# Kernel optimization log

Hardware: AMD Instinct MI355X
Metric: run time of the kernel (lower is better)

The kernel has to match this reference:

```python
import jax, jax.numpy as jnp
import numpy as np

B, T, C, H = 4, 1024, 1024, 16
HS = C // H  # head_size = 64
EPS = 1e-5


def layer_norm(x, w, b):
    mu = jnp.mean(x, axis=-1, keepdims=True)
    var = jnp.mean(jnp.square(x - mu), axis=-1, keepdims=True)
    return (x - mu) * jax.lax.rsqrt(var + EPS) * w + b


def setup_inputs() -> dict:
    key = jax.random.key(0)
    ks = jax.random.split(key, 12)
    s = 0.02
    return {
        "x": jax.random.normal(ks[0], (B, T, C), jnp.float32),
        "ln1_w": jnp.ones((C,), jnp.float32),
        "ln1_b": jnp.zeros((C,), jnp.float32),
        "Wk": jax.random.normal(ks[1], (H, C, HS), jnp.float32) * s,
        "Wq": jax.random.normal(ks[2], (H, C, HS), jnp.float32) * s,
        "Wv": jax.random.normal(ks[3], (H, C, HS), jnp.float32) * s,
        "Wo": jax.random.normal(ks[4], (C, C), jnp.float32) * s,
        "bo": jnp.zeros((C,), jnp.float32),
        "ln2_w": jnp.ones((C,), jnp.float32),
        "ln2_b": jnp.zeros((C,), jnp.float32),
        "W1": jax.random.normal(ks[5], (C, 4 * C), jnp.float32) * s,
        "b1": jnp.zeros((4 * C,), jnp.float32),
        "prelu_a": jnp.asarray(0.25, jnp.float32),
        "W2": jax.random.normal(ks[6], (4 * C, C), jnp.float32) * s,
        "b2": jnp.zeros((C,), jnp.float32),
    }


def reference(x, ln1_w, ln1_b, Wk, Wq, Wv, Wo, bo, ln2_w, ln2_b, W1, b1, prelu_a, W2, b2):
    # --- self-attention branch (pre-LN) ---
    h = layer_norm(x, ln1_w, ln1_b)  # [B,T,C]
    k = jnp.einsum('btc,hcd->bhtd', h, Wk)
    q = jnp.einsum('btc,hcd->bhtd', h, Wq)
    v = jnp.einsum('btc,hcd->bhtd', h, Wv)
    # NOTE: source computes k @ q^T (not q @ k^T) scaled by n_embd**-0.5
    wei = jnp.einsum('bhtd,bhsd->bhts', k, q) * (C ** -0.5)  # [B,H,T,T]
    causal = jnp.tril(jnp.ones((T, T), bool))
    wei = jnp.where(causal, wei, -jnp.inf)
    wei = jax.nn.softmax(wei, axis=-1)
    out = jnp.einsum('bhts,bhsd->bthd', wei, v).reshape(B, T, C)
    out = out @ Wo + bo
    x = x + out
    # --- feed-forward branch (pre-LN) ---
    h2 = layer_norm(x, ln2_w, ln2_b)
    f = h2 @ W1 + b1
    f = jnp.where(f > 0, f, prelu_a * f)  # PReLU, single scalar param
    f = f @ W2 + b2
    return x + f
```

## Files before the change

kernel.cpp:

```cpp
#include <hip/hip_runtime.h>


typedef __bf16 bf16_t;
typedef __attribute__((ext_vector_type(8))) __bf16 bfx8;
typedef __attribute__((ext_vector_type(4))) __bf16 bfx4;
typedef __attribute__((ext_vector_type(4))) float f32x4;
typedef __attribute__((ext_vector_type(8))) unsigned short u16x8;
typedef unsigned int u32;

#define MFMA_BF16(a, b, c) __builtin_amdgcn_mfma_f32_16x16x32_bf16((a), (b), (c), 0, 0, 0)
#define GLOAD_LDS16(g, l)                                                     \
  __builtin_amdgcn_global_load_lds((__attribute__((address_space(1))) void*)(g), \
                                   (__attribute__((address_space(3))) void*)(l), 16, 0, 0)
#define BARX()                      \
  __builtin_amdgcn_s_barrier();     \
  __builtin_amdgcn_sched_barrier(0)
#define VMW6()                                     \
  asm volatile("s_waitcnt vmcnt(6)" ::: "memory"); \
  __builtin_amdgcn_sched_barrier(0)
#define VMW0()                                     \
  asm volatile("s_waitcnt vmcnt(0)" ::: "memory"); \
  __builtin_amdgcn_sched_barrier(0)

__global__ __launch_bounds__(256) void ln_kernel(const float* __restrict__ x,
                                                 const float* __restrict__ w,
                                                 const float* __restrict__ b,
                                                 bf16_t* __restrict__ out) {
  const int row = blockIdx.x;
  const int tid = threadIdx.x;
  const float4 v = reinterpret_cast<const float4*>(x + (size_t)row * 1024)[tid];
  float s = v.x + v.y + v.z + v.w;
  float s2 = v.x * v.x + v.y * v.y + v.z * v.z + v.w * v.w;
#pragma unroll
  for (int off = 1; off < 64; off <<= 1) {
    s += __shfl_xor(s, off);
    s2 += __shfl_xor(s2, off);
  }
  __shared__ float red[8];
  const int wv = tid >> 6;
  if ((tid & 63) == 0) {
    red[wv] = s;
    red[4 + wv] = s2;
  }
  __syncthreads();
  s = red[0] + red[1] + red[2] + red[3];
  s2 = red[4] + red[5] + red[6] + red[7];
  const float mu = s * (1.0f / 1024.0f);
  const float rs = rsqrtf(s2 * (1.0f / 1024.0f) - mu * mu + 1e-5f);
  const float4 wv4 = reinterpret_cast<const float4*>(w)[tid];
  const float4 bv4 = reinterpret_cast<const float4*>(b)[tid];
  bfx4 o;
  o[0] = (bf16_t)((v.x - mu) * rs * wv4.x + bv4.x);
  o[1] = (bf16_t)((v.y - mu) * rs * wv4.y + bv4.y);
  o[2] = (bf16_t)((v.z - mu) * rs * wv4.z + bv4.z);
  o[3] = (bf16_t)((v.w - mu) * rs * wv4.w + bv4.w);
  reinterpret_cast<bfx4*>(out + (size_t)row * 1024)[tid] = o;
}

__device__ __forceinline__ void tc_body(const float* __restrict__ in,
                                        bf16_t* __restrict__ out, int K, int N, int k0,
                                        int n0, float (*tile)[65], int t) {
  const int rl = t >> 4, cl = (t & 15) * 4;
#pragma unroll
  for (int p = 0; p < 4; ++p) {
    const int r = p * 16 + rl;
    const float4 v = *reinterpret_cast<const float4*>(in + (size_t)(k0 + r) * N + n0 + cl);
    tile[r][cl] = v.x;
    tile[r][cl + 1] = v.y;
    tile[r][cl + 2] = v.z;
    tile[r][cl + 3] = v.w;
  }
  __syncthreads();
#pragma unroll
  for (int p = 0; p < 2; ++p) {
    const int idx = p * 256 + t;
    const int n = idx >> 3, kc = (idx & 7) * 8;
    bfx8 o;
#pragma unroll
    for (int i = 0; i < 8; ++i) o[i] = (bf16_t)tile[kc + i][n];
    *reinterpret_cast<bfx8*>(out + (size_t)(n0 + n) * K + k0 + kc) = o;
  }
}

__global__ __launch_bounds__(256) void transpose_cast(const float* __restrict__ in,
                                                      bf16_t* __restrict__ out, int K,
                                                      int N) {
  __shared__ float tile[64][65];
  tc_body(in, out, K, N, blockIdx.x * 64, blockIdx.y * 64, tile, threadIdx.x);
}

__global__ __launch_bounds__(256) void transpose_qkv(const float* __restrict__ Wq,
                                                     const float* __restrict__ Wk,
                                                     const float* __restrict__ Wv,
                                                     bf16_t* __restrict__ out) {
  __shared__ float tile[64][65];
  const int z = blockIdx.y;
  const int sel = z >> 4, h = z & 15;
  const float* in = ((sel == 0) ? Wq : (sel == 1) ? Wk : Wv) + h * 65536;
  bf16_t* o = out + (size_t)sel * 1048576 + h * 65536;
  tc_body(in, o, 1024, 64, blockIdx.x * 64, 0, tile, threadIdx.x);
}

enum { EPI_QKV = 0, EPI_WO = 1 };

template <int EPI, int BM, int BN, int NT>
__global__ __launch_bounds__(NT, 2) void gemm_bt(
    const bf16_t* __restrict__ A, const bf16_t* __restrict__ BT,
    const float* __restrict__ bias, const float* __restrict__ res,
    float* __restrict__ outf, bf16_t* __restrict__ ob0, bf16_t* __restrict__ ob1,
    bf16_t* __restrict__ ob2, int K, int N) {
  constexpr int WM = 2;
  constexpr int WN = NT / 64 / WM;
  constexpr int MF = BM / WM / 16;
  constexpr int NF = BN / WN / 16;
  constexpr int ACH = BM * 64 / (NT * 8);
  constexpr int BCH = BN * 64 / (NT * 8);
  constexpr int LOADS = ACH + BCH;
  static_assert(LOADS == 8 || LOADS == 6, "add a vmcnt case");
  __shared__ __align__(16) bf16_t sA[2][BM * 64];
  __shared__ __align__(16) bf16_t sB[2][BN * 64];
  const int tid = threadIdx.x;
  const int lane = tid & 63;
  const int w = tid >> 6;
  const int wr = w / WN, wc = w % WN;
  const int g = lane >> 4, l15 = lane & 15;
  const int row0 = blockIdx.x * BM, col0 = blockIdx.y * BN;
  const int rowbase = row0 + wr * (BM / WM);
  const int colbase = wc * (BN / WN);

  f32x4 acc[MF][NF] = {};

  auto stage = [&](int k0, int buf) {
#pragma unroll
    for (int j = 0; j < ACH; ++j) {
      const int chunk = j * NT + tid;
      const int r = chunk >> 3, c = chunk & 7;
      GLOAD_LDS16(A + (size_t)(row0 + r) * K + k0 + ((c ^ (r & 7)) * 8),
                  sA[buf] + chunk * 8);
    }
#pragma unroll
    for (int j = 0; j < BCH; ++j) {
      const int chunk = j * NT + tid;
      const int r = chunk >> 3, c = chunk & 7;
      GLOAD_LDS16(BT + (size_t)(col0 + r) * K + k0 + ((c ^ (r & 7)) * 8),
                  sB[buf] + chunk * 8);
    }
  };

  stage(0, 0);
  const int nk = K >> 6;
  for (int t = 0; t < nk; ++t) {
    const int cur = t & 1;
    if (t + 1 < nk) {
      stage((t + 1) << 6, cur ^ 1);
      __builtin_amdgcn_sched_barrier(0);
      if constexpr (LOADS == 8)
        asm volatile("s_waitcnt vmcnt(8)" ::: "memory");
      else
        asm volatile("s_waitcnt vmcnt(6)" ::: "memory");
    } else {
      __builtin_amdgcn_sched_barrier(0);
      asm volatile("s_waitcnt vmcnt(0)" ::: "memory");
    }
    __builtin_amdgcn_s_barrier();
    __builtin_amdgcn_sched_barrier(0);
    const bf16_t* __restrict__ pA = sA[cur];
    const bf16_t* __restrict__ pB = sB[cur];
#pragma unroll
    for (int kk = 0; kk < 2; ++kk) {
      bfx8 af[MF], bfr[NF];
#pragma unroll
      for (int m = 0; m < MF; ++m) {
        const int r = wr * (BM / WM) + m * 16 + l15;
        const int c = (kk * 4 + g) ^ (r & 7);
        af[m] = *reinterpret_cast<const bfx8*>(pA + r * 64 + c * 8);
      }
#pragma unroll
      for (int n = 0; n < NF; ++n) {
        const int r = colbase + n * 16 + l15;
        const int c = (kk * 4 + g) ^ (r & 7);
        bfr[n] = *reinterpret_cast<const bfx8*>(pB + r * 64 + c * 8);
      }
#pragma unroll
      for (int m = 0; m < MF; ++m)
#pragma unroll
        for (int n = 0; n < NF; ++n) acc[m][n] = MFMA_BF16(af[m], bfr[n], acc[m][n]);
    }
    __builtin_amdgcn_sched_barrier(0);
    __builtin_amdgcn_s_barrier();
  }

#pragma unroll
  for (int m = 0; m < MF; ++m) {
#pragma unroll
    for (int n = 0; n < NF; ++n) {
#pragma unroll
      for (int j = 0; j < 4; ++j) {
        const int row = rowbase + m * 16 + (g << 2) + j;
        const int col = col0 + colbase + n * 16 + l15;
        const float v = acc[m][n][j];
        if (EPI == EPI_QKV) {
          const int sel = col >> 10;
          const int h = (col >> 6) & 15, d = col & 63;
          const int bb = row >> 10, t = row & 1023;
          bf16_t* dst = (sel == 0) ? ob0 : (sel == 1) ? ob1 : ob2;
          dst[((size_t)(bb * 16 + h) * 1024 + t) * 64 + d] = (bf16_t)v;
        } else {
          outf[(size_t)row * N + col] = v + bias[col] + res[(size_t)row * N + col];
        }
      }
    }
  }
}

__device__ __forceinline__ void stageA8(const bf16_t* __restrict__ A, int Ks, int row0,
                                        int k0, int mh, bf16_t* dst, int tid) {
#pragma unroll
  for (int g2 = 0; g2 < 2; ++g2) {
    const int band = g2 * 128 + mh * 64;
    const int row = band + (tid >> 3);
    GLOAD_LDS16(A + (size_t)(row0 + row) * Ks + k0 + (((tid & 7) ^ (row & 7)) * 8),
                dst + band * 64 + tid * 8);
  }
}

__device__ __forceinline__ void stageB8(const bf16_t* __restrict__ BT, int Ks, int col0,
                                        int k0, int nh, bf16_t* dst, int tid) {
#pragma unroll
  for (int g2 = 0; g2 < 2; ++g2) {
    const int rho = g2 * 64 + (tid >> 3);
    const int grow = (rho >> 5) * 64 + nh * 32 + (rho & 31);
    GLOAD_LDS16(BT + (size_t)(col0 + grow) * Ks + k0 + (((tid & 7) ^ (rho & 7)) * 8),
                dst + nh * 8192 + g2 * 4096 + tid * 8);
  }
}

template <int MH, int NH, bool LOADA>
__device__ __forceinline__ void quad8(const bf16_t* __restrict__ pA,
                                      const bf16_t* __restrict__ pB, int wr, int wc,
                                      int l15, int g, bfx8 (&af)[4][2],
                                      f32x4 (&acc)[8][4]) {
  if (LOADA) {
#pragma unroll
    for (int i = 0; i < 4; ++i) {
      const int r = wr * 128 + (MH * 4 + i) * 16 + l15;
#pragma unroll
      for (int kk = 0; kk < 2; ++kk)
        af[i][kk] =
            *reinterpret_cast<const bfx8*>(pA + r * 64 + (((kk * 4 + g) ^ (r & 7)) * 8));
    }
  }
  bfx8 bfr[2][2];
#pragma unroll
  for (int i = 0; i < 2; ++i) {
    const int rho = wc * 32 + i * 16 + l15;
#pragma unroll
    for (int kk = 0; kk < 2; ++kk)
      bfr[i][kk] = *reinterpret_cast<const bfx8*>(pB + NH * 8192 + rho * 64 +
                                                  (((kk * 4 + g) ^ (rho & 7)) * 8));
  }
  __builtin_amdgcn_s_setprio(1);
#pragma unroll
  for (int i = 0; i < 4; ++i)
#pragma unroll
    for (int jn = 0; jn < 2; ++jn)
#pragma unroll
      for (int kk = 0; kk < 2; ++kk)
        acc[MH * 4 + i][NH * 2 + jn] =
            MFMA_BF16(af[i][kk], bfr[jn][kk], acc[MH * 4 + i][NH * 2 + jn]);
  __builtin_amdgcn_s_setprio(0);
}

template <bool PRELU>
__global__ __launch_bounds__(512, 2) void gemm_8ph(
    const bf16_t* __restrict__ A, const bf16_t* __restrict__ BT,
    const float* __restrict__ bias, const float* __restrict__ prelu,
    bf16_t* __restrict__ outb, int Ks, int Klen, int N, size_t zstride) {
  __shared__ __align__(16) bf16_t sA[2][256 * 64];
  __shared__ __align__(16) bf16_t sB[2][256 * 64];
  const int tid = threadIdx.x;
  const int lane = tid & 63;
  const int w = tid >> 6;
  const int wr = w >> 2, wc = w & 3;
  const int g = lane >> 4, l15 = lane & 15;
  const int row0 = blockIdx.x * 256, col0 = blockIdx.y * 256;
  const int koff = blockIdx.z * Klen;

  f32x4 acc[8][4] = {};
  bfx8 af[4][2];

  stageA8(A, Ks, row0, koff, 0, sA[0], tid);
  stageB8(BT, Ks, col0, koff, 0, sB[0], tid);
  stageB8(BT, Ks, col0, koff, 1, sB[0], tid);
  stageA8(A, Ks, row0, koff, 1, sA[0], tid);
  stageA8(A, Ks, row0, koff + 64, 0, sA[1], tid);
  stageB8(BT, Ks, col0, koff + 64, 0, sB[1], tid);

  const int nt = Klen >> 7;
  for (int j = 0; j < nt; ++j) {
    const bool more = (j + 1 < nt);
    const int ku1 = koff + ((2 * j + 1) << 6), k2 = koff + ((2 * j + 2) << 6),
              k3 = koff + ((2 * j + 3) << 6);
    BARX();
    stageB8(BT, Ks, col0, ku1, 1, sB[1], tid);
    VMW6();
    BARX();
    quad8<0, 0, true>(sA[0], sB[0], wr, wc, l15, g, af, acc);
    BARX();
    stageA8(A, Ks, row0, ku1, 1, sA[1], tid);
    quad8<0, 1, false>(sA[0], sB[0], wr, wc, l15, g, af, acc);
    BARX();
    if (more) stageA8(A, Ks, row0, k2, 0, sA[0], tid);
    quad8<1, 0, true>(sA[0], sB[0], wr, wc, l15, g, af, acc);
    BARX();
    if (more) stageB8(BT, Ks, col0, k2, 0, sB[0], tid);
    quad8<1, 1, false>(sA[0], sB[0], wr, wc, l15, g, af, acc);
    BARX();
    if (more) {
      stageB8(BT, Ks, col0, k2, 1, sB[0], tid);
      VMW6();
    } else {
      VMW0();
    }
    BARX();
    quad8<0, 0, true>(sA[1], sB[1], wr, wc, l15, g, af, acc);
    BARX();
    if (more) stageA8(A, Ks, row0, k2, 1, sA[0], tid);
    quad8<0, 1, false>(sA[1], sB[1], wr, wc, l15, g, af, acc);
    BARX();
    if (more) stageA8(A, Ks, row0, k3, 0, sA[1], tid);
    quad8<1, 0, true>(sA[1], sB[1], wr, wc, l15, g, af, acc);
    BARX();
    if (more) stageB8(BT, Ks, col0, k3, 0, sB[1], tid);
    quad8<1, 1, false>(sA[1], sB[1], wr, wc, l15, g, af, acc);
  }

  bf16_t* o = outb + (size_t)blockIdx.z * zstride;
  const float pa = PRELU ? prelu[0] : 0.0f;
#pragma unroll
  for (int m = 0; m < 8; ++m) {
#pragma unroll
    for (int n = 0; n < 4; ++n) {
#pragma unroll
      for (int j = 0; j < 4; ++j) {
        const int row = row0 + wr * 128 + m * 16 + (g << 2) + j;
        const int col = col0 + wc * 64 + n * 16 + l15;
        float t = acc[m][n][j];
        if (PRELU) {
          t += bias[col];
          t = (t > 0.0f) ? t : pa * t;
        }
        o[(size_t)row * N + col] = (bf16_t)t;
      }
    }
  }
}

__global__ __launch_bounds__(256) void reduce_mlp2(const bf16_t* __restrict__ part,
                                                   const float* __restrict__ b2,
                                                   float* __restrict__ out) {
  const int idx = (blockIdx.x * 256 + threadIdx.x) * 8;
  const int col = idx & 1023;
  float a[8];
  {
    const float4 o0 = *reinterpret_cast<const float4*>(out + idx);
    const float4 o1 = *reinterpret_cast<const float4*>(out + idx + 4);
    const float4 b0 = *reinterpret_cast<const float4*>(b2 + col);
    const float4 b1 = *reinterpret_cast<const float4*>(b2 + col + 4);
    a[0] = o0.x + b0.x; a[1] = o0.y + b0.y; a[2] = o0.z + b0.z; a[3] = o0.w + b0.w;
    a[4] = o1.x + b1.x; a[5] = o1.y + b1.y; a[6] = o1.z + b1.z; a[7] = o1.w + b1.w;
  }
#pragma unroll
  for (int s = 0; s < 4; ++s) {
    const u16x8 p = *reinterpret_cast<const u16x8*>(part + (size_t)s * 4194304 + idx);
#pragma unroll
    for (int i = 0; i < 8; ++i) a[i] += __uint_as_float((u32)p[i] << 16);
  }
  float4 r0{a[0], a[1], a[2], a[3]}, r1{a[4], a[5], a[6], a[7]};
  *reinterpret_cast<float4*>(out + idx) = r0;
  *reinterpret_cast<float4*>(out + idx + 4) = r1;
}

__global__ __launch_bounds__(256) void attn_kernel(const bf16_t* __restrict__ kproj,
                                                   const bf16_t* __restrict__ qproj,
                                                   const bf16_t* __restrict__ vproj,
                                                   bf16_t* __restrict__ att) {
  __shared__ __align__(16) bf16_t sK[2][64 * 64];
  __shared__ __align__(16) bf16_t sVt[2][64 * 64];
  __shared__ __align__(16) bf16_t sP[4][16 * 64];
  const int tid = threadIdx.x, lane = tid & 63, w = tid >> 6;
  const int g = lane >> 4, l15 = lane & 15;
  const int bh = blockIdx.y;
  const size_t head = (size_t)bh * (1024 * 64);
  const int b = bh >> 4, h = bh & 15;
  const int vrow = 2 * (tid >> 3);
  const int vdb = tid & 7;

  for (int half = 0; half < 2; ++half) {
    const int tb = half ? (15 - (int)blockIdx.x) : (int)blockIdx.x;
    const int t0 = tb * 64;
    const int nsb = tb + 1;

    __syncthreads();

    bfx8 aq0, aq1;
    {
      const bf16_t* qrow = kproj + head + (size_t)(t0 + w * 16 + l15) * 64 + g * 8;
      aq0 = *reinterpret_cast<const bfx8*>(qrow);
      aq1 = *reinterpret_cast<const bfx8*>(qrow + 32);
    }

    {
#pragma unroll
      for (int j = 0; j < 2; ++j) {
        const int chunk = j * 256 + tid;
        const int r = chunk >> 3, c = chunk & 7;
        const int cs = c ^ (r & 7);
        GLOAD_LDS16(qproj + head + (size_t)r * 64 + cs * 8, sK[0] + chunk * 8);
      }
      const bf16_t* vp = vproj + head + (size_t)vrow * 64 + vdb * 8;
      const u16x8 v0 = *reinterpret_cast<const u16x8*>(vp);
      const u16x8 v1 = *reinterpret_cast<const u16x8*>(vp + 64);
#pragma unroll
      for (int i = 0; i < 8; ++i) {
        const int d = vdb * 8 + i;
        const int cc = ((vrow >> 3) ^ i ^ vdb) & 7;
        const u32 pk = ((u32)v1[i] << 16) | (u32)v0[i];
        *reinterpret_cast<u32*>(sVt[0] + d * 64 + cc * 8 + (vrow & 7)) = pk;
      }
    }
    __syncthreads();

    f32x4 accO[4] = {};
    float mrun[4], lrun[4];
#pragma unroll
    for (int j = 0; j < 4; ++j) {
      mrun[j] = -1e30f;
      lrun[j] = 0.0f;
    }

    for (int sb = 0; sb < nsb; ++sb) {
      const int cur = sb & 1;
      const bool pf = (sb + 1 < nsb);
      const bool diag = (sb == tb);
      u16x8 v0n, v1n;
      if (pf) {
        const int s0n = (sb + 1) * 64;
#pragma unroll
        for (int j = 0; j < 2; ++j) {
          const int chunk = j * 256 + tid;
          const int r = chunk >> 3, c = chunk & 7;
          const int cs = c ^ (r & 7);
          GLOAD_LDS16(qproj + head + (size_t)(s0n + r) * 64 + cs * 8, sK[cur ^ 1] + chunk * 8);
        }
        const bf16_t* vp = vproj + head + (size_t)(s0n + vrow) * 64 + vdb * 8;
        v0n = *reinterpret_cast<const u16x8*>(vp);
        v1n = *reinterpret_cast<const u16x8*>(vp + 64);
      }

      f32x4 accS[4] = {};
      const bf16_t* sKc = sK[cur];
#pragma unroll
      for (int kk = 0; kk < 2; ++kk) {
        const bfx8 aq = kk ? aq1 : aq0;
#pragma unroll
        for (int n = 0; n < 4; ++n) {
          const int r = n * 16 + l15;
          const int c = (kk * 4 + g) ^ (r & 7);
          const bfx8 bk = *reinterpret_cast<const bfx8*>(sKc + r * 64 + c * 8);
          accS[n] = MFMA_BF16(aq, bk, accS[n]);
        }
      }

      const int rbase = t0 + w * 16 + (g << 2);
      const int cbase = sb * 64 + l15;
#pragma unroll
      for (int j = 0; j < 4; ++j) {
        const int t = rbase + j;
        float mx = -1e30f;
        if (diag) {
#pragma unroll
          for (int n = 0; n < 4; ++n) {
            float v = accS[n][j] * 0.03125f;
            v = ((cbase + n * 16) <= t) ? v : -1e30f;
            accS[n][j] = v;
            mx = fmaxf(mx, v);
          }
        } else {
#pragma unroll
          for (int n = 0; n < 4; ++n) {
            const float v = accS[n][j] * 0.03125f;
            accS[n][j] = v;
            mx = fmaxf(mx, v);
          }
        }
        mx = fmaxf(mx, __shfl_xor(mx, 1));
        mx = fmaxf(mx, __shfl_xor(mx, 2));
        mx = fmaxf(mx, __shfl_xor(mx, 4));
        mx = fmaxf(mx, __shfl_xor(mx, 8));
        const float mnew = fmaxf(mrun[j], mx);
        const float al = __expf(mrun[j] - mnew);
        float rsum = 0.0f;
#pragma unroll
        for (int n = 0; n < 4; ++n) {
          const float p = __expf(accS[n][j] - mnew);
          accS[n][j] = p;
          rsum += p;
        }
        rsum += __shfl_xor(rsum, 1);
        rsum += __shfl_xor(rsum, 2);
        rsum += __shfl_xor(rsum, 4);
        rsum += __shfl_xor(rsum, 8);
        lrun[j] = lrun[j] * al + rsum;
        mrun[j] = mnew;
#pragma unroll
        for (int n = 0; n < 4; ++n) accO[n][j] *= al;
      }

      bf16_t* sPw = sP[w];
#pragma unroll
      for (int n = 0; n < 4; ++n)
#pragma unroll
        for (int j = 0; j < 4; ++j) {
          const int r = (g << 2) + j;
          const int s = n * 16 + l15;
          const int cc = (s >> 3) ^ (r & 7);
          sPw[r * 64 + cc * 8 + (s & 7)] = (bf16_t)accS[n][j];
        }

      const bf16_t* sVc = sVt[cur];
#pragma unroll
      for (int kk = 0; kk < 2; ++kk) {
        bfx8 ap;
        {
          const int r = l15;
          const int c = (kk * 4 + g) ^ (r & 7);
          ap = *reinterpret_cast<const bfx8*>(sPw + r * 64 + c * 8);
        }
#pragma unroll
        for (int n = 0; n < 4; ++n) {
          const int d = n * 16 + l15;
          const int c = (kk * 4 + g) ^ (d & 7) ^ ((d >> 3) & 7);
          const bfx8 bv = *reinterpret_cast<const bfx8*>(sVc + d * 64 + c * 8);
          accO[n] = MFMA_BF16(ap, bv, accO[n]);
        }
      }

      if (pf) {
#pragma unroll
        for (int i = 0; i < 8; ++i) {
          const int d = vdb * 8 + i;
          const int cc = ((vrow >> 3) ^ i ^ vdb) & 7;
          const u32 pk = ((u32)v1n[i] << 16) | (u32)v0n[i];
          *reinterpret_cast<u32*>(sVt[cur ^ 1] + d * 64 + cc * 8 + (vrow & 7)) = pk;
        }
      }
      __syncthreads();
    }

#pragma unroll
    for (int j = 0; j < 4; ++j) {
      const float inv = 1.0f / lrun[j];
      const int t = t0 + w * 16 + (g << 2) + j;
#pragma unroll
      for (int n = 0; n < 4; ++n) {
        const int d = n * 16 + l15;
        att[((size_t)(b * 1024 + t)) * 1024 + h * 64 + d] = (bf16_t)(accO[n][j] * inv);
      }
    }
  }
}

extern "C" void kernel_launch(void* const* d_in, const int* in_sizes, int n_in,
                              void* d_out, int out_size, void* d_ws, size_t ws_size,
                              hipStream_t stream) {
  (void)in_sizes; (void)n_in; (void)out_size; (void)ws_size;
  const float* x = (const float*)d_in[0];
  const float* ln1w = (const float*)d_in[1];
  const float* ln1b = (const float*)d_in[2];
  const float* Wk = (const float*)d_in[3];
  const float* Wq = (const float*)d_in[4];
  const float* Wv = (const float*)d_in[5];
  const float* Wo = (const float*)d_in[6];
  const float* bo = (const float*)d_in[7];
  const float* ln2w = (const float*)d_in[8];
  const float* ln2b = (const float*)d_in[9];
  const float* W1 = (const float*)d_in[10];
  const float* b1 = (const float*)d_in[11];
  const float* pa = (const float*)d_in[12];
  const float* W2 = (const float*)d_in[13];
  const float* b2 = (const float*)d_in[14];
  float* out = (float*)d_out;
  char* ws = (char*)d_ws;
  const size_t MB = 1ull << 20;
  bf16_t* h1 = (bf16_t*)(ws + 0 * MB);
  bf16_t* h2 = (bf16_t*)(ws + 8 * MB);
  bf16_t* qb = (bf16_t*)(ws + 16 * MB);
  bf16_t* kb = (bf16_t*)(ws + 24 * MB);
  bf16_t* vb = (bf16_t*)(ws + 32 * MB);
  bf16_t* attb = (bf16_t*)(ws + 40 * MB);
  bf16_t* fbuf = (bf16_t*)(ws + 48 * MB);
  bf16_t* part = (bf16_t*)(ws + 16 * MB);
  bf16_t* WqkvT = (bf16_t*)(ws + 80 * MB);
  bf16_t* WoT = (bf16_t*)(ws + 86 * MB);
  bf16_t* W1T = (bf16_t*)(ws + 88 * MB);
  bf16_t* W2T = (bf16_t*)(ws + 96 * MB);

  transpose_qkv<<<dim3(16, 48), 256, 0, stream>>>(Wq, Wk, Wv, WqkvT);
  transpose_cast<<<dim3(16, 16), 256, 0, stream>>>(Wo, WoT, 1024, 1024);
  transpose_cast<<<dim3(16, 64), 256, 0, stream>>>(W1, W1T, 1024, 4096);
  transpose_cast<<<dim3(64, 16), 256, 0, stream>>>(W2, W2T, 4096, 1024);

  ln_kernel<<<4096, 256, 0, stream>>>(x, ln1w, ln1b, h1);
  gemm_bt<EPI_QKV, 256, 256, 512><<<dim3(16, 12), 512, 0, stream>>>(
      h1, WqkvT, nullptr, nullptr, nullptr, qb, kb, vb, 1024, 3072);
  attn_kernel<<<dim3(8, 64), 256, 0, stream>>>(kb, qb, vb, attb);
  gemm_bt<EPI_WO, 64, 128, 256><<<dim3(64, 8), 256, 0, stream>>>(
      attb, WoT, bo, x, out, nullptr, nullptr, nullptr, 1024, 1024);
  ln_kernel<<<4096, 256, 0, stream>>>(out, ln2w, ln2b, h2);
  gemm_8ph<true><<<dim3(16, 16, 1), 512, 0, stream>>>(h2, W1T, b1, pa, fbuf, 1024, 1024,
                                                      4096, 0);
  gemm_8ph<false><<<dim3(16, 4, 4), 512, 0, stream>>>(fbuf, W2T, nullptr, nullptr, part,
                                                      4096, 1024, 1024, 4194304);
  reduce_mlp2<<<2048, 256, 0, stream>>>(part, b2, out);
}
```

Baseline: 219.1 us.

## Reschedule attention blocks longest-first with lazy softmax rescaling and exp2

The attention kernel no longer pairs two query tiles per block. It launches 1024 blocks ordered so the longest causal rows are dispatched first, which is meant to improve load balance and occupancy. The online softmax now works in the exp2 domain by folding log2(e) into the scale. It rescales the running max only when the new max exceeds the old one by more than a threshold, and it defers the row-sum cross-lane reductions to the end. This cuts shuffles and exponentials per key tile, but it allows unnormalized values up to 2^8 before the final division, which carries some numeric risk.

Result: faster. 204.5 us (-6.7%).

```diff
diff --git a/kernel.cpp b/kernel.cpp
--- a/kernel.cpp
+++ b/kernel.cpp
@@ -390,183 +390,195 @@
   __shared__ __align__(16) bf16_t sP[4][16 * 64];
   const int tid = threadIdx.x, lane = tid & 63, w = tid >> 6;
   const int g = lane >> 4, l15 = lane & 15;
-  const int bh = blockIdx.y;
+  const int f = blockIdx.x;
+  const int tb = 15 - ((f >> 3) >> 3);
+  const int bh = (((f >> 3) & 7) << 3) + (f & 7);
   const size_t head = (size_t)bh * (1024 * 64);
   const int b = bh >> 4, h = bh & 15;
   const int vrow = 2 * (tid >> 3);
   const int vdb = tid & 7;
-
-  for (int half = 0; half < 2; ++half) {
-    const int tb = half ? (15 - (int)blockIdx.x) : (int)blockIdx.x;
-    const int t0 = tb * 64;
-    const int nsb = tb + 1;
-
-    __syncthreads();
-
-    bfx8 aq0, aq1;
-    {
-      const bf16_t* qrow = kproj + head + (size_t)(t0 + w * 16 + l15) * 64 + g * 8;
-      aq0 = *reinterpret_cast<const bfx8*>(qrow);
-      aq1 = *reinterpret_cast<const bfx8*>(qrow + 32);
-    }
-
-    {
+  const int t0 = tb * 64;
+  const int nsb = tb + 1;
+
+  bfx8 aq0, aq1;
+  {
+    const bf16_t* qrow = kproj + head + (size_t)(t0 + w * 16 + l15) * 64 + g * 8;
+    aq0 = *reinterpret_cast<const bfx8*>(qrow);
+    aq1 = *reinterpret_cast<const bfx8*>(qrow + 32);
+  }
+
+  {
+#pragma unroll
+    for (int j = 0; j < 2; ++j) {
+      const int chunk = j * 256 + tid;
+      const int r = chunk >> 3, c = chunk & 7;
+      const int cs = c ^ (r & 7);
+      GLOAD_LDS16(qproj + head + (size_t)r * 64 + cs * 8, sK[0] + chunk * 8);
+    }
+    const bf16_t* vp = vproj + head + (size_t)vrow * 64 + vdb * 8;
+    const u16x8 v0 = *reinterpret_cast<const u16x8*>(vp);
+    const u16x8 v1 = *reinterpret_cast<const u16x8*>(vp + 64);
+#pragma unroll
+    for (int i = 0; i < 8; ++i) {
+      const int d = vdb * 8 + i;
+      const int cc = ((vrow >> 3) ^ i ^ vdb) & 7;
+      const u32 pk = ((u32)v1[i] << 16) | (u32)v0[i];
+      *reinterpret_cast<u32*>(sVt[0] + d * 64 + cc * 8 + (vrow & 7)) = pk;
+    }
+  }
+  __syncthreads();
+
+  f32x4 accO[4] = {};
+  float m2[4], lp[4];
+#pragma unroll
+  for (int j = 0; j < 4; ++j) {
+    m2[j] = -1e30f;
+    lp[j] = 0.0f;
+  }
+
+  for (int sb = 0; sb < nsb; ++sb) {
+    const int cur = sb & 1;
+    const bool pf = (sb + 1 < nsb);
+    const bool diag = (sb == tb);
+    u16x8 v0n, v1n;
+    if (pf) {
+      const int s0n = (sb + 1) * 64;
 #pragma unroll
       for (int j = 0; j < 2; ++j) {
         const int chunk = j * 256 + tid;
         const int r = chunk >> 3, c = chunk & 7;
         const int cs = c ^ (r & 7);
-        GLOAD_LDS16(qproj + head + (size_t)r * 64 + cs * 8, sK[0] + chunk * 8);
-      }
-      const bf16_t* vp = vproj + head + (size_t)vrow * 64 + vdb * 8;
-      const u16x8 v0 = *reinterpret_cast<const u16x8*>(vp);
-      const u16x8 v1 = *reinterpret_cast<const u16x8*>(vp + 64);
-#pragma unroll
-      for (int i = 0; i < 8; ++i) {
-        const int d = vdb * 8 + i;
-        const int cc = ((vrow >> 3) ^ i ^ vdb) & 7;
-        const u32 pk = ((u32)v1[i] << 16) | (u32)v0[i];
-        *reinterpret_cast<u32*>(sVt[0] + d * 64 + cc * 8 + (vrow & 7)) = pk;
-      }
-    }
-    __syncthreads();
-
-    f32x4 accO[4] = {};
-    float mrun[4], lrun[4];
+        GLOAD_LDS16(qproj + head + (size_t)(s0n + r) * 64 + cs * 8, sK[cur ^ 1] + chunk * 8);
+      }
+      const bf16_t* vp = vproj + head + (size_t)(s0n + vrow) * 64 + vdb * 8;
+      v0n = *reinterpret_cast<const u16x8*>(vp);
+      v1n = *reinterpret_cast<const u16x8*>(vp + 64);
+    }
+
+    f32x4 accS[4] = {};
+    const bf16_t* sKc = sK[cur];
+#pragma unroll
+    for (int kk = 0; kk < 2; ++kk) {
+      const bfx8 aq = kk ? aq1 : aq0;
+#pragma unroll
+      for (int n = 0; n < 4; ++n) {
+        const int r = n * 16 + l15;
+        const int c = (kk * 4 + g) ^ (r & 7);
+        const bfx8 bk = *reinterpret_cast<const bfx8*>(sKc + r * 64 + c * 8);
+        accS[n] = MFMA_BF16(aq, bk, accS[n]);
+      }
+    }
+
+    constexpr float SC = 0.04508056640625f;
+    const int rbase = t0 + w * 16 + (g << 2);
+    const int cbase = sb * 64 + l15;
+    float rmx[4];
+    float dmax = -3e38f;
 #pragma unroll
     for (int j = 0; j < 4; ++j) {
-      mrun[j] = -1e30f;
-      lrun[j] = 0.0f;
-    }
-
-    for (int sb = 0; sb < nsb; ++sb) {
-      const int cur = sb & 1;
-      const bool pf = (sb + 1 < nsb);
-      const bool diag = (sb == tb);
-      u16x8 v0n, v1n;
-      if (pf) {
-        const int s0n = (sb + 1) * 64;
-#pragma unroll
-        for (int j = 0; j < 2; ++j) {
-          const int chunk = j * 256 + tid;
-          const int r = chunk >> 3, c = chunk & 7;
-          const int cs = c ^ (r & 7);
-          GLOAD_LDS16(qproj + head + (size_t)(s0n + r) * 64 + cs * 8, sK[cur ^ 1] + chunk * 8);
+      const int t = rbase + j;
+      float mx = -1e30f;
+      if (diag) {
+#pragma unroll
+        for (int n = 0; n < 4; ++n) {
+          float v = accS[n][j] * SC;
+          v = ((cbase + n * 16) <= t) ? v : -1e30f;
+          accS[n][j] = v;
+          mx = fmaxf(mx, v);
         }
-        const bf16_t* vp = vproj + head + (size_t)(s0n + vrow) * 64 + vdb * 8;
-        v0n = *reinterpret_cast<const u16x8*>(vp);
-        v1n = *reinterpret_cast<const u16x8*>(vp + 64);
-      }
-
-      f32x4 accS[4] = {};
-      const bf16_t* sKc = sK[cur];
-#pragma unroll
-      for (int kk = 0; kk < 2; ++kk) {
-        const bfx8 aq = kk ? aq1 : aq0;
+      } else {
 #pragma unroll
         for (int n = 0; n < 4; ++n) {
-          const int r = n * 16 + l15;
-          const int c = (kk * 4 + g) ^ (r & 7);
-          const bfx8 bk = *reinterpret_cast<const bfx8*>(sKc + r * 64 + c * 8);
-          accS[n] = MFMA_BF16(aq, bk, accS[n]);
+          const float v = accS[n][j] * SC;
+          accS[n][j] = v;
+          mx = fmaxf(mx, v);
         }
       }
-
-      const int rbase = t0 + w * 16 + (g << 2);
-      const int cbase = sb * 64 + l15;
+      rmx[j] = mx;
+      dmax = fmaxf(dmax, mx - m2[j]);
+    }
+    if (__any(dmax > 8.0f)) {
 #pragma unroll
       for (int j = 0; j < 4; ++j) {
-        const int t = rbase + j;
-        float mx = -1e30f;
-        if (diag) {
-#pragma unroll
-          for (int n = 0; n < 4; ++n) {
-            float v = accS[n][j] * 0.03125f;
-            v = ((cbase + n * 16) <= t) ? v : -1e30f;
-            accS[n][j] = v;
-            mx = fmaxf(mx, v);
-          }
-        } else {
-#pragma unroll
-          for (int n = 0; n < 4; ++n) {
-            const float v = accS[n][j] * 0.03125f;
-            accS[n][j] = v;
-            mx = fmaxf(mx, v);
-          }
-        }
+        float mx = rmx[j];
         mx = fmaxf(mx, __shfl_xor(mx, 1));
         mx = fmaxf(mx, __shfl_xor(mx, 2));
         mx = fmaxf(mx, __shfl_xor(mx, 4));
         mx = fmaxf(mx, __shfl_xor(mx, 8));
-        const float mnew = fmaxf(mrun[j], mx);
-        const float al = __expf(mrun[j] - mnew);
-        float rsum = 0.0f;
-#pragma unroll
-        for (int n = 0; n < 4; ++n) {
-          const float p = __expf(accS[n][j] - mnew);
-          accS[n][j] = p;
-          rsum += p;
-        }
-        rsum += __shfl_xor(rsum, 1);
-        rsum += __shfl_xor(rsum, 2);
-        rsum += __shfl_xor(rsum, 4);
-        rsum += __shfl_xor(rsum, 8);
-        lrun[j] = lrun[j] * al + rsum;
-        mrun[j] = mnew;
+        const float mnew = fmaxf(m2[j], mx);
+        const float al = __builtin_amdgcn_exp2f(m2[j] - mnew);
+        m2[j] = mnew;
+        lp[j] *= al;
 #pragma unroll
         for (int n = 0; n < 4; ++n) accO[n][j] *= al;
       }
-
-      bf16_t* sPw = sP[w];
-#pragma unroll
-      for (int n = 0; n < 4; ++n)
-#pragma unroll
-        for (int j = 0; j < 4; ++j) {
-          const int r = (g << 2) + j;
-          const int s = n * 16 + l15;
-          const int cc = (s >> 3) ^ (r & 7);
-          sPw[r * 64 + cc * 8 + (s & 7)] = (bf16_t)accS[n][j];
-        }
-
-      const bf16_t* sVc = sVt[cur];
-#pragma unroll
-      for (int kk = 0; kk < 2; ++kk) {
-        bfx8 ap;
-        {
-          const int r = l15;
-          const int c = (kk * 4 + g) ^ (r & 7);
-          ap = *reinterpret_cast<const bfx8*>(sPw + r * 64 + c * 8);
-        }
-#pragma unroll
-        for (int n = 0; n < 4; ++n) {
-          const int d = n * 16 + l15;
-          const int c = (kk * 4 + g) ^ (d & 7) ^ ((d >> 3) & 7);
-          const bfx8 bv = *reinterpret_cast<const bfx8*>(sVc + d * 64 + c * 8);
-          accO[n] = MFMA_BF16(ap, bv, accO[n]);
-        }
-      }
-
-      if (pf) {
-#pragma unroll
-        for (int i = 0; i < 8; ++i) {
-          const int d = vdb * 8 + i;
-          const int cc = ((vrow >> 3) ^ i ^ vdb) & 7;
-          const u32 pk = ((u32)v1n[i] << 16) | (u32)v0n[i];
-          *reinterpret_cast<u32*>(sVt[cur ^ 1] + d * 64 + cc * 8 + (vrow & 7)) = pk;
-        }
-      }
-      __syncthreads();
-    }
-
+    }
 #pragma unroll
     for (int j = 0; j < 4; ++j) {
-      const float inv = 1.0f / lrun[j];
-      const int t = t0 + w * 16 + (g << 2) + j;
+      float s = 0.0f;
+#pragma unroll
+      for (int n = 0; n < 4; ++n) {
+        const float p = __builtin_amdgcn_exp2f(accS[n][j] - m2[j]);
+        accS[n][j] = p;
+        s += p;
+      }
+      lp[j] += s;
+    }
+
+    bf16_t* sPw = sP[w];
+#pragma unroll
+    for (int n = 0; n < 4; ++n)
+#pragma unroll
+      for (int j = 0; j < 4; ++j) {
+        const int r = (g << 2) + j;
+        const int s = n * 16 + l15;
+        const int cc = (s >> 3) ^ (r & 7);
+        sPw[r * 64 + cc * 8 + (s & 7)] = (bf16_t)accS[n][j];
+      }
+
+    const bf16_t* sVc = sVt[cur];
+#pragma unroll
+    for (int kk = 0; kk < 2; ++kk) {
+      bfx8 ap;
+      {
+        const int r = l15;
+        const int c = (kk * 4 + g) ^ (r & 7);
+        ap = *reinterpret_cast<const bfx8*>(sPw + r * 64 + c * 8);
+      }
 #pragma unroll
       for (int n = 0; n < 4; ++n) {
         const int d = n * 16 + l15;
-        att[((size_t)(b * 1024 + t)) * 1024 + h * 64 + d] = (bf16_t)(accO[n][j] * inv);
-      }
+        const int c = (kk * 4 + g) ^ (d & 7) ^ ((d >> 3) & 7);
+        const bfx8 bv = *reinterpret_cast<const bfx8*>(sVc + d * 64 + c * 8);
+        accO[n] = MFMA_BF16(ap, bv, accO[n]);
+      }
+    }
+
+    if (pf) {
+#pragma unroll
+      for (int i = 0; i < 8; ++i) {
+        const int d = vdb * 8 + i;
+        const int cc = ((vrow >> 3) ^ i ^ vdb) & 7;
+        const u32 pk = ((u32)v1n[i] << 16) | (u32)v0n[i];
+        *reinterpret_cast<u32*>(sVt[cur ^ 1] + d * 64 + cc * 8 + (vrow & 7)) = pk;
+      }
+    }
+    __syncthreads();
+  }
+
+#pragma unroll
+  for (int j = 0; j < 4; ++j) {
+    float l = lp[j];
+    l += __shfl_xor(l, 1);
+    l += __shfl_xor(l, 2);
+    l += __shfl_xor(l, 4);
+    l += __shfl_xor(l, 8);
+    const float inv = 1.0f / l;
+    const int t = t0 + w * 16 + (g << 2) + j;
+#pragma unroll
+    for (int n = 0; n < 4; ++n) {
+      const int d = n * 16 + l15;
+      att[((size_t)(b * 1024 + t)) * 1024 + h * 64 + d] = (bf16_t)(accO[n][j] * inv);
     }
   }
 }
@@ -614,7 +626,7 @@
   ln_kernel<<<4096, 256, 0, stream>>>(x, ln1w, ln1b, h1);
   gemm_bt<EPI_QKV, 256, 256, 512><<<dim3(16, 12), 512, 0, stream>>>(
       h1, WqkvT, nullptr, nullptr, nullptr, qb, kb, vb, 1024, 3072);
-  attn_kernel<<<dim3(8, 64), 256, 0, stream>>>(kb, qb, vb, attb);
+  attn_kernel<<<1024, 256, 0, stream>>>(kb, qb, vb, attb);
   gemm_bt<EPI_WO, 64, 128, 256><<<dim3(64, 8), 256, 0, stream>>>(
       attb, WoT, bo, x, out, nullptr, nullptr, nullptr, 1024, 1024);
   ln_kernel<<<4096, 256, 0, stream>>>(out, ln2w, ln2b, h2);
```
